# Kernel tuning notes

Hardware: AMD Instinct MI355X
Metric: run time of the kernel (lower is better)

## Reference

```python
import jax, jax.numpy as jnp
import numpy as np

GATE_THRESH = 0.4
LN_EPS = 1e-5
NORM_EPS = 1e-12  # torch F.normalize eps


def setup_inputs() -> dict:
    key = jax.random.key(0)
    ks = jax.random.split(key, 8)
    B, L, H, V = 64, 1024, 64, 32000
    s = lambda k, shape, scale: (jax.random.normal(k, shape, jnp.float32) * scale)
    return {
        "seq": jax.random.randint(ks[0], (B, L), 0, V),
        "embed": s(ks[1], (V, H), 0.02),
        "W1": s(ks[2], (H, 2 * H), 0.05), "b1": jnp.zeros((2 * H,), jnp.float32),
        "W2": s(ks[3], (2 * H, H), 0.05), "b2": jnp.zeros((H,), jnp.float32),
        "gamma": jnp.ones((H,), jnp.float32), "beta": jnp.zeros((H,), jnp.float32),
        "kpW": s(ks[4], (H, H), 0.1),
        "rpW": s(ks[5], (H, H), 0.1), "rpb": jnp.zeros((H,), jnp.float32),
        "outW": s(ks[6], (H, V), 0.05), "outb": jnp.zeros((V,), jnp.float32),
    }


def reference(seq, embed, W1, b1, W2, b2, gamma, beta, kpW, rpW, rpb, outW, outb):
    # embed + FF residual + LayerNorm
    h = embed[seq]                                        # (B,L,H)
    ffo = jax.nn.relu(h @ W1 + b1) @ W2 + b2
    x = h + ffo
    mu = x.mean(-1, keepdims=True)
    var = x.var(-1, keepdims=True)                        # biased, like torch LN
    h = (x - mu) * jax.lax.rsqrt(var + LN_EPS) * gamma + beta

    k_all = h @ kpW                                       # kp projection for all t, (B,L,H)
    B, L, H = h.shape

    def step(M, k):                                       # M: (B,H,H), k: (B,H)
        kn = k / jnp.maximum(jnp.linalg.norm(k, axis=-1, keepdims=True), NORM_EPS)
        vp = jnp.einsum('bij,bj->bi', M, kn)
        err = k - vp
        gate = (jnp.linalg.norm(err, axis=-1) >= GATE_THRESH * jnp.linalg.norm(k, axis=-1)).astype(k.dtype)
        Delta = gate[:, None, None] * err[:, :, None] * kn[:, None, :]
        return M + Delta, None                            # use_ema=False -> plain accumulation

    M0 = jnp.zeros((B, H, H), h.dtype)
    M, _ = jax.lax.scan(step, M0, jnp.swapaxes(k_all[:, :-1], 0, 1))  # scan over L-1 steps

    q = k_all[:, -1]                                      # query from last token
    read = jnp.einsum('bij,bj->bi', M, q)
    return (read @ rpW + rpb) @ outW + outb               # (B,V)
```

## Files before the change

### kernel.cpp

```cpp
#include <hip/hip_runtime.h>
#include <hip/hip_bf16.h>

#define HDIM 64
#define LSEQ 1024
#define NB 64
#define NV 32000
#define CC 32
#define NCH 32
#define NT (NB * LSEQ)

template<int CTRL>
__device__ __forceinline__ float dpp_red(float x) {
  int y = __builtin_amdgcn_update_dpp(0, __float_as_int(x), CTRL, 0xF, 0xF, true);
  return x + __int_as_float(y);
}
__device__ __forceinline__ float quad_sum(float x) {
  x = dpp_red<0xB1>(x);
  x = dpp_red<0x4E>(x);
  return x;
}
__device__ __forceinline__ float wave_sum(float x) {
  x = dpp_red<0xB1>(x);
  x = dpp_red<0x4E>(x);
  x = dpp_red<0x141>(x);
  x = dpp_red<0x140>(x);
  float a = __int_as_float(__builtin_amdgcn_readlane(__float_as_int(x), 0));
  float b = __int_as_float(__builtin_amdgcn_readlane(__float_as_int(x), 16));
  float c = __int_as_float(__builtin_amdgcn_readlane(__float_as_int(x), 32));
  float d = __int_as_float(__builtin_amdgcn_readlane(__float_as_int(x), 48));
  return (a + b) + (c + d);
}

__global__ __launch_bounds__(256) void transpose_w(const float* __restrict__ W1,
    const float* __restrict__ kpW, float* __restrict__ W1T, float* __restrict__ kpWT)
{
  const int tid = blockIdx.x * 256 + threadIdx.x;
  if (tid < 8192) { const int c = tid >> 6, j = tid & 63; W1T[tid] = W1[j * 128 + c]; }
  else { const int e = tid - 8192; const int i = e >> 6, j = e & 63; kpWT[e] = kpW[j * 64 + i]; }
}

__global__ __launch_bounds__(256, 1) void tok4(
    const int* __restrict__ seq, const float* __restrict__ embed,
    const float* __restrict__ W1T, const float* __restrict__ b1,
    const float* __restrict__ W2, const float* __restrict__ b2,
    const float* __restrict__ gamma, const float* __restrict__ beta,
    const float* __restrict__ kpWT, float* __restrict__ kallT,
    float* __restrict__ thr2_all, float* __restrict__ inv_all)
{
  const int tok = blockIdx.x * 256 + threadIdx.x;
  const int row = seq[tok];
  float h[64], x[64];
  const float4* ep = (const float4*)(embed + (size_t)row * HDIM);
  #pragma unroll
  for (int q = 0; q < 16; ++q) {
    const float4 v = ep[q];
    h[4*q] = v.x; h[4*q+1] = v.y; h[4*q+2] = v.z; h[4*q+3] = v.w;
  }
  #pragma unroll
  for (int j = 0; j < 64; ++j) x[j] = h[j] + b2[j];

  for (int c = 0; c < 128; ++c) {
    const float* w1r = W1T + c * 64;
    float a0 = 0.f, a1 = 0.f, a2 = 0.f, a3 = 0.f;
    #pragma unroll
    for (int j = 0; j < 64; j += 4) {
      a0 = fmaf(h[j],   w1r[j],   a0);
      a1 = fmaf(h[j+1], w1r[j+1], a1);
      a2 = fmaf(h[j+2], w1r[j+2], a2);
      a3 = fmaf(h[j+3], w1r[j+3], a3);
    }
    const float y = fmaxf(b1[c] + ((a0 + a1) + (a2 + a3)), 0.f);
    const float* w2r = W2 + c * 64;
    #pragma unroll
    for (int j = 0; j < 64; ++j) x[j] = fmaf(y, w2r[j], x[j]);
  }

  float s0=0.f,s1=0.f,s2=0.f,s3=0.f,q0=0.f,q1=0.f,q2=0.f,q3=0.f;
  #pragma unroll
  for (int j = 0; j < 64; j += 4) {
    s0 += x[j]; s1 += x[j+1]; s2 += x[j+2]; s3 += x[j+3];
    q0 = fmaf(x[j],   x[j],   q0); q1 = fmaf(x[j+1], x[j+1], q1);
    q2 = fmaf(x[j+2], x[j+2], q2); q3 = fmaf(x[j+3], x[j+3], q3);
  }
  const float mu  = ((s0+s1)+(s2+s3)) * (1.f/64.f);
  const float var = ((q0+q1)+(q2+q3)) * (1.f/64.f) - mu * mu;
  const float rs  = rsqrtf(var + 1e-5f);
  #pragma unroll
  for (int j = 0; j < 64; ++j) h[j] = (x[j] - mu) * rs * gamma[j] + beta[j];

  float nk2 = 0.f;
  for (int i = 0; i < 64; ++i) {
    const float* kr = kpWT + i * 64;
    float c0=0.f,c1=0.f,c2=0.f,c3=0.f;
    #pragma unroll
    for (int j = 0; j < 64; j += 4) {
      c0 = fmaf(h[j],   kr[j],   c0);
      c1 = fmaf(h[j+1], kr[j+1], c1);
      c2 = fmaf(h[j+2], kr[j+2], c2);
      c3 = fmaf(h[j+3], kr[j+3], c3);
    }
    const float ki = (c0 + c1) + (c2 + c3);
    nk2 = fmaf(ki, ki, nk2);
    kallT[(size_t)i * NT + tok] = ki;
  }
  thr2_all[tok] = 0.16f * nk2;
  inv_all[tok]  = 1.f / fmaxf(sqrtf(nk2), 1e-12f);
}

__global__ __launch_bounds__(64) void gram2(const float* __restrict__ kallT,
    const float* __restrict__ inv_all, float* __restrict__ Gg)
{
  const int bi = blockIdx.x;
  const int b = bi >> 5, ch = bi & 31;
  const int l = threadIdx.x;
  const int t0 = (l & 7) * 4, s0 = (l >> 3) * 4;
  const size_t gb = (size_t)b * LSEQ + ch * CC;
  float g00=0,g01=0,g02=0,g03=0, g10=0,g11=0,g12=0,g13=0;
  float g20=0,g21=0,g22=0,g23=0, g30=0,g31=0,g32=0,g33=0;
  for (int j = 0; j < 64; ++j) {
    const float* rowp = kallT + (size_t)j * NT + gb;
    const float4 a = *(const float4*)(rowp + t0);
    const float4 c = *(const float4*)(rowp + s0);
    g00=fmaf(a.x,c.x,g00); g01=fmaf(a.x,c.y,g01); g02=fmaf(a.x,c.z,g02); g03=fmaf(a.x,c.w,g03);
    g10=fmaf(a.y,c.x,g10); g11=fmaf(a.y,c.y,g11); g12=fmaf(a.y,c.z,g12); g13=fmaf(a.y,c.w,g13);
    g20=fmaf(a.z,c.x,g20); g21=fmaf(a.z,c.y,g21); g22=fmaf(a.z,c.z,g22); g23=fmaf(a.z,c.w,g23);
    g30=fmaf(a.w,c.x,g30); g31=fmaf(a.w,c.y,g31); g32=fmaf(a.w,c.z,g32); g33=fmaf(a.w,c.w,g33);
  }
  const float4 it = *(const float4*)(inv_all + gb + t0);
  const float4 is = *(const float4*)(inv_all + gb + s0);
  float* Go = Gg + (size_t)bi * (CC * CC);
  float4 o;
  o.x=g00*it.x*is.x; o.y=g01*it.x*is.y; o.z=g02*it.x*is.z; o.w=g03*it.x*is.w;
  *(float4*)(Go + (t0+0)*CC + s0) = o;
  o.x=g10*it.y*is.x; o.y=g11*it.y*is.y; o.z=g12*it.y*is.z; o.w=g13*it.y*is.w;
  *(float4*)(Go + (t0+1)*CC + s0) = o;
  o.x=g20*it.z*is.x; o.y=g21*it.z*is.y; o.z=g22*it.z*is.z; o.w=g23*it.z*is.w;
  *(float4*)(Go + (t0+2)*CC + s0) = o;
  o.x=g30*it.w*is.x; o.y=g31*it.w*is.y; o.z=g32*it.w*is.z; o.w=g33*it.w*is.w;
  *(float4*)(Go + (t0+3)*CC + s0) = o;
}

__global__ __launch_bounds__(192, 1) void scan6(
    const float* __restrict__ kallT, const float* __restrict__ thr2_all,
    const float* __restrict__ inv_all, const float* __restrict__ Gg,
    float* __restrict__ readv)
{
  __shared__ float kS[3][CC * 68];
  __shared__ float GS[2][CC * CC];
  __shared__ float rS[CC * 64];
  __shared__ float cstS[CC * 64];
  __shared__ float thr2S[2][CC];
  __shared__ float invS[3][CC];

  const int b = blockIdx.x, tid = threadIdx.x;
  const int w = tid >> 6, l = tid & 63;
  const int A = l >> 2, B4 = l & 3;
  const int r0 = 32 * (w - 1) + 2 * A;
  const int jb = 16 * B4;
  const size_t gbase = (size_t)b * LSEQ;

  float M0[16], M1[16], acc[32];
  #pragma unroll
  for (int q = 0; q < 16; ++q) { M0[q] = 0.f; M1[q] = 0.f; }

#define A2_SLICE(KB, IB, T0) do {                                              \
    _Pragma("unroll")                                                          \
    for (int t = (T0); t < (T0) + 8; ++t) {                                    \
      const float* kr = &kS[KB][t * 68 + jb];                                  \
      float p0a=0.f,p0b=0.f,p1a=0.f,p1b=0.f;                                   \
      _Pragma("unroll")                                                        \
      for (int q2 = 0; q2 < 4; ++q2) {                                         \
        const float4 kv = ((const float4*)kr)[q2];                             \
        p0a = fmaf(M0[4*q2+0], kv.x, p0a); p0b = fmaf(M0[4*q2+1], kv.y, p0b);  \
        p0a = fmaf(M0[4*q2+2], kv.z, p0a); p0b = fmaf(M0[4*q2+3], kv.w, p0b);  \
        p1a = fmaf(M1[4*q2+0], kv.x, p1a); p1b = fmaf(M1[4*q2+1], kv.y, p1b);  \
        p1a = fmaf(M1[4*q2+2], kv.z, p1a); p1b = fmaf(M1[4*q2+3], kv.w, p1b);  \
      }                                                                        \
      float p0 = quad_sum(p0a + p0b);                                          \
      float p1 = quad_sum(p1a + p1b);                                          \
      const float iv = invS[IB][t];                                            \
      if (B4 == 0) *(float2*)&rS[t * 64 + r0] = make_float2(p0 * iv, p1 * iv); \
    }                                                                          \
  } while (0)

#define C_SLICE(KB, IB, S0) do {                                               \
    _Pragma("unroll")                                                          \
    for (int s = (S0); s < (S0) + 8; ++s) {                                    \
      const float2 cc2 = *(const float2*)&cstS[s * 64 + r0];                   \
      const float iv = invS[IB][s];                                            \
      const float c0 = cc2.x * iv, c1 = cc2.y * iv;                            \
      const float* kr = &kS[KB][s * 68 + jb];                                  \
      _Pragma("unroll")                                                        \
      for (int q2 = 0; q2 < 4; ++q2) {                                         \
        const float4 kv = ((const float4*)kr)[q2];                             \
        M0[4*q2+0] = fmaf(c0, kv.x, M0[4*q2+0]); M0[4*q2+1] = fmaf(c0, kv.y, M0[4*q2+1]); \
        M0[4*q2+2] = fmaf(c0, kv.z, M0[4*q2+2]); M0[4*q2+3] = fmaf(c0, kv.w, M0[4*q2+3]); \
        M1[4*q2+0] = fmaf(c1, kv.x, M1[4*q2+0]); M1[4*q2+1] = fmaf(c1, kv.y, M1[4*q2+1]); \
        M1[4*q2+2] = fmaf(c1, kv.z, M1[4*q2+2]); M1[4*q2+3] = fmaf(c1, kv.w, M1[4*q2+3]); \
      }                                                                        \
    }                                                                          \
  } while (0)

#define B_SLICE(Q, CBUF, CGI, LASTCH) do {                                     \
    const int t0_ = 8 * (Q);                                                   \
    _Pragma("unroll")                                                          \
    for (int i = 0; i < 8; ++i) {                                              \
      const int u = t0_ + i;                                                   \
      acc[u] += kS[CBUF][u * 68 + l] - rS[u * 64 + l];                         \
    }                                                                          \
    const float4 tha = ((const float4*)&thr2S[CGI][t0_])[0];                   \
    const float4 thb = ((const float4*)&thr2S[CGI][t0_])[1];                   \
    const float th8[8] = {tha.x,tha.y,tha.z,tha.w, thb.x,thb.y,thb.z,thb.w};   \
    _Pragma("unroll")                                                          \
    for (int i = 0; i < 8; ++i) {                                              \
      const int t = t0_ + i;                                                   \
      float g[32];                                                             \
      const float4* gp = (const float4*)&GS[CGI][t * 32];                      \
      _Pragma("unroll")                                                        \
      for (int r = 0; r < 8; ++r) {                                            \
        const float4 v = gp[r];                                                \
        g[4*r]=v.x; g[4*r+1]=v.y; g[4*r+2]=v.z; g[4*r+3]=v.w;                  \
      }                                                                        \
      const float err = acc[t];                                                \
      const float ne2 = wave_sum(err * err);                                   \
      bool gate = (ne2 >= th8[i]);                                             \
      if ((LASTCH) && t == CC - 1) gate = false;                               \
      const float c = gate ? err : 0.f;                                        \
      cstS[t * 64 + l] = c;                                                    \
      _Pragma("unroll")                                                        \
      for (int u = 0; u < 32; ++u) acc[u] = fmaf(-g[u], c, acc[u]);            \
    }                                                                          \
  } while (0)

  if (w < 2) {
    const float* src = kallT + (size_t)l * NT + gbase + w * 16;
    #pragma unroll
    for (int q = 0; q < 4; ++q) {
      const float4 v = ((const float4*)src)[q];
      const int t0 = w * 16 + q * 4;
      kS[0][(t0+0)*68 + l] = v.x; kS[0][(t0+1)*68 + l] = v.y;
      kS[0][(t0+2)*68 + l] = v.z; kS[0][(t0+3)*68 + l] = v.w;
    }
  } else {
    const float4* gsrc = (const float4*)(Gg + (size_t)b * NCH * (CC * CC));
    #pragma unroll
    for (int q = 0; q < 4; ++q) ((float4*)GS[0])[q * 64 + l] = gsrc[q * 64 + l];
    if (l < CC) thr2S[0][l] = thr2_all[gbase + l];
    else        invS[0][l - CC] = inv_all[gbase + (l - CC)];
  }
  __syncthreads();

  for (int ch = 0; ch < NCH; ++ch) {
    const int cb = ch % 3, pb = (ch + 2) % 3, nb = (ch + 1) % 3;
    const int cg = ch & 1, ng = 1 - cg;
    const bool lastch = (ch == NCH - 1);

    if (w == 0) {
      #pragma unroll
      for (int u = 0; u < 32; ++u) acc[u] = 0.f;
      if (!lastch) {
        const float* src = kallT + (size_t)l * NT + gbase + (ch + 1) * CC;
        #pragma unroll
        for (int q = 0; q < 8; ++q) {
          const float4 v = ((const float4*)src)[q];
          const int t0 = q * 4;
          kS[nb][(t0+0)*68 + l] = v.x; kS[nb][(t0+1)*68 + l] = v.y;
          kS[nb][(t0+2)*68 + l] = v.z; kS[nb][(t0+3)*68 + l] = v.w;
        }
        const float4* gsrc = (const float4*)(Gg + ((size_t)b * NCH + ch + 1) * (CC * CC));
        #pragma unroll
        for (int q = 0; q < 4; ++q) ((float4*)GS[ng])[q * 64 + l] = gsrc[q * 64 + l];
        if (l < CC) thr2S[ng][l] = thr2_all[gbase + (ch + 1) * CC + l];
        else        invS[nb][l - CC] = inv_all[gbase + (ch + 1) * CC + (l - CC)];
      }
    } else {
      if (ch > 0) C_SLICE(pb, pb, 24);
      A2_SLICE(cb, cb, 0);
    }
    __syncthreads();

    if (w == 0) B_SLICE(0, cb, cg, lastch);
    else        A2_SLICE(cb, cb, 8);
    __syncthreads();
    if (w == 0) B_SLICE(1, cb, cg, lastch);
    else        A2_SLICE(cb, cb, 16);
    __syncthreads();
    if (w == 0) B_SLICE(2, cb, cg, lastch);
    else { A2_SLICE(cb, cb, 24); C_SLICE(cb, cb, 0); }
    __syncthreads();
    if (w == 0) B_SLICE(3, cb, cg, lastch);
    else { C_SLICE(cb, cb, 8); C_SLICE(cb, cb, 16); }
    __syncthreads();
  }

  {
    constexpr int fb = (NCH - 1) % 3;
    if (w > 0) {
      C_SLICE(fb, fb, 24);
      const float* kr = &kS[fb][(CC - 1) * 68 + jb];
      float p0a=0.f,p0b=0.f,p1a=0.f,p1b=0.f;
      #pragma unroll
      for (int q2 = 0; q2 < 4; ++q2) {
        const float4 kv = ((const float4*)kr)[q2];
        p0a = fmaf(M0[4*q2+0], kv.x, p0a); p0b = fmaf(M0[4*q2+1], kv.y, p0b);
        p0a = fmaf(M0[4*q2+2], kv.z, p0a); p0b = fmaf(M0[4*q2+3], kv.w, p0b);
        p1a = fmaf(M1[4*q2+0], kv.x, p1a); p1b = fmaf(M1[4*q2+1], kv.y, p1b);
        p1a = fmaf(M1[4*q2+2], kv.z, p1a); p1b = fmaf(M1[4*q2+3], kv.w, p1b);
      }
      float d0 = quad_sum(p0a + p0b);
      float d1 = quad_sum(p1a + p1b);
      if (B4 == 0) *(float2*)&readv[b * 64 + r0] = make_float2(d0, d1);
    }
  }
#undef A2_SLICE
#undef C_SLICE
#undef B_SLICE
}

__global__ __launch_bounds__(64) void rproj_kernel(const float* __restrict__ readv,
    const float* __restrict__ rpW, const float* __restrict__ rpb, float* __restrict__ r2T)
{
  const int b = blockIdx.x, i = threadIdx.x;
  const float* rv = readv + b * 64;
  float acc = rpb[i];
  #pragma unroll
  for (int j = 0; j < 64; ++j)
    acc = fmaf(rv[j], rpW[j * 64 + i], acc);
  r2T[i * 64 + b] = acc;
}

__global__ __launch_bounds__(256, 1) void out_kernel(const float* __restrict__ r2T,
    const float* __restrict__ outW, const float* __restrict__ outb,
    float* __restrict__ out)
{
  const int v = blockIdx.x * 256 + threadIdx.x;
  float acc[64];
  #pragma unroll
  for (int b = 0; b < 64; ++b) acc[b] = 0.f;
  for (int k = 0; k < 64; ++k) {
    const float wv = outW[(size_t)k * NV + v];
    const float* rr = r2T + k * 64;
    #pragma unroll
    for (int b = 0; b < 64; ++b)
      acc[b] = fmaf(rr[b], wv, acc[b]);
  }
  const float ob = outb[v];
  #pragma unroll
  for (int b = 0; b < 64; ++b)
    out[(size_t)b * NV + v] = acc[b] + ob;
}

extern "C" void kernel_launch(void* const* d_in, const int* in_sizes, int n_in,
                              void* d_out, int out_size, void* d_ws, size_t ws_size,
                              hipStream_t stream)
{
  const int*   seq   = (const int*)d_in[0];
  const float* embed = (const float*)d_in[1];
  const float* W1    = (const float*)d_in[2];
  const float* b1    = (const float*)d_in[3];
  const float* W2    = (const float*)d_in[4];
  const float* b2    = (const float*)d_in[5];
  const float* gam   = (const float*)d_in[6];
  const float* bet   = (const float*)d_in[7];
  const float* kpW   = (const float*)d_in[8];
  const float* rpW   = (const float*)d_in[9];
  const float* rpb   = (const float*)d_in[10];
  const float* outW  = (const float*)d_in[11];
  const float* outb  = (const float*)d_in[12];
  float* out = (float*)d_out;

  float* ws = (float*)d_ws;
  float* kallT = ws;
  float* G     = kallT + (size_t)HDIM * NT;
  float* thr2  = G     + (size_t)NB * NCH * CC * CC;
  float* inv   = thr2  + NT;
  float* readv = inv   + NT;
  float* r2T   = readv + NB * HDIM;
  float* W1T   = r2T   + NB * HDIM;
  float* kpWT  = W1T   + 8192;

  hipLaunchKernelGGL(transpose_w, dim3(48), dim3(256), 0, stream, W1, kpW, W1T, kpWT);
  hipLaunchKernelGGL(tok4, dim3(256), dim3(256), 0, stream,
                     seq, embed, W1T, b1, W2, b2, gam, bet, kpWT, kallT, thr2, inv);
  hipLaunchKernelGGL(gram2, dim3(NB * NCH), dim3(64), 0, stream, kallT, inv, G);
  hipLaunchKernelGGL(scan6, dim3(NB), dim3(192), 0, stream, kallT, thr2, inv, G, readv);
  hipLaunchKernelGGL(rproj_kernel, dim3(NB), dim3(64), 0, stream, readv, rpW, rpb, r2T);
  hipLaunchKernelGGL(out_kernel, dim3(NV / 256), dim3(256), 0, stream, r2T, outW, outb, out);
}
```

Measured before the change: 485.5 us.

## Pipeline gate reduction in scan slice and shrink output kernel blocks

Restructures the per-step gating loop in the sequential scan. The next step's error is updated and reduced before the remaining accumulator updates, so the wave reduction latency overlaps with the FMA work. Gram rows are double-buffered and loaded one step ahead, and updates skip triangular entries that no longer matter. The wave sum now uses row-broadcast DPP with a single readlane instead of four readlanes. Separately, the output projection kernel uses 128-thread blocks to spread its 250 blocks across more CUs. This adds register pressure and more complex control flow in the scan.

```diff
diff --git a/kernel.cpp b/kernel.cpp
--- a/kernel.cpp
+++ b/kernel.cpp
@@ -19,16 +19,14 @@
   x = dpp_red<0x4E>(x);
   return x;
 }
-__device__ __forceinline__ float wave_sum(float x) {
+__device__ __forceinline__ float wave_sum63(float x) {
   x = dpp_red<0xB1>(x);
   x = dpp_red<0x4E>(x);
   x = dpp_red<0x141>(x);
   x = dpp_red<0x140>(x);
-  float a = __int_as_float(__builtin_amdgcn_readlane(__float_as_int(x), 0));
-  float b = __int_as_float(__builtin_amdgcn_readlane(__float_as_int(x), 16));
-  float c = __int_as_float(__builtin_amdgcn_readlane(__float_as_int(x), 32));
-  float d = __int_as_float(__builtin_amdgcn_readlane(__float_as_int(x), 48));
-  return (a + b) + (c + d);
+  x = dpp_red<0x142>(x);
+  x = dpp_red<0x143>(x);
+  return x;
 }
 
 __global__ __launch_bounds__(256) void transpose_w(const float* __restrict__ W1,
@@ -203,32 +201,49 @@
 
 #define B_SLICE(Q, CBUF, CGI, LASTCH) do {                                     \
     const int t0_ = 8 * (Q);                                                   \
+    float kr_[8], rr_[8];                                                      \
     _Pragma("unroll")                                                          \
     for (int i = 0; i < 8; ++i) {                                              \
-      const int u = t0_ + i;                                                   \
-      acc[u] += kS[CBUF][u * 68 + l] - rS[u * 64 + l];                         \
+      kr_[i] = kS[CBUF][(t0_ + i) * 68 + l];                                   \
+      rr_[i] = rS[(t0_ + i) * 64 + l];                                         \
     }                                                                          \
     const float4 tha = ((const float4*)&thr2S[CGI][t0_])[0];                   \
     const float4 thb = ((const float4*)&thr2S[CGI][t0_])[1];                   \
     const float th8[8] = {tha.x,tha.y,tha.z,tha.w, thb.x,thb.y,thb.z,thb.w};   \
+    float g2_[2][32];                                                          \
+    _Pragma("unroll")                                                          \
+    for (int q = (t0_ + 1) >> 2; q < 8; ++q) {                                 \
+      const float4 v = ((const float4*)&GS[CGI][t0_ * 32])[q];                 \
+      g2_[0][4*q+0] = v.x; g2_[0][4*q+1] = v.y;                                \
+      g2_[0][4*q+2] = v.z; g2_[0][4*q+3] = v.w;                                \
+    }                                                                          \
+    float err_ = acc[t0_] + kr_[0] - rr_[0];                                   \
+    float red_ = wave_sum63(err_ * err_);                                      \
     _Pragma("unroll")                                                          \
     for (int i = 0; i < 8; ++i) {                                              \
       const int t = t0_ + i;                                                   \
-      float g[32];                                                             \
-      const float4* gp = (const float4*)&GS[CGI][t * 32];                      \
+      if (i < 7) {                                                             \
+        _Pragma("unroll")                                                      \
+        for (int q = (t + 2) >> 2; q < 8; ++q) {                               \
+          const float4 v = ((const float4*)&GS[CGI][(t + 1) * 32])[q];         \
+          g2_[(i+1)&1][4*q+0] = v.x; g2_[(i+1)&1][4*q+1] = v.y;                \
+          g2_[(i+1)&1][4*q+2] = v.z; g2_[(i+1)&1][4*q+3] = v.w;                \
+        }                                                                      \
+      }                                                                        \
+      const float ne2_ = __int_as_float(                                       \
+          __builtin_amdgcn_readlane(__float_as_int(red_), 63));                \
+      bool gate_ = (ne2_ >= th8[i]);                                           \
+      if ((LASTCH) && t == CC - 1) gate_ = false;                              \
+      const float c = gate_ ? err_ : 0.f;                                      \
+      cstS[t * 64 + l] = c;                                                    \
+      if (i < 7) {                                                             \
+        acc[t + 1] = fmaf(-g2_[i & 1][t + 1], c, acc[t + 1]);                  \
+        err_ = acc[t + 1] + kr_[i + 1] - rr_[i + 1];                           \
+        red_ = wave_sum63(err_ * err_);                                        \
+      }                                                                        \
       _Pragma("unroll")                                                        \
-      for (int r = 0; r < 8; ++r) {                                            \
-        const float4 v = gp[r];                                                \
-        g[4*r]=v.x; g[4*r+1]=v.y; g[4*r+2]=v.z; g[4*r+3]=v.w;                  \
-      }                                                                        \
-      const float err = acc[t];                                                \
-      const float ne2 = wave_sum(err * err);                                   \
-      bool gate = (ne2 >= th8[i]);                                             \
-      if ((LASTCH) && t == CC - 1) gate = false;                               \
-      const float c = gate ? err : 0.f;                                        \
-      cstS[t * 64 + l] = c;                                                    \
-      _Pragma("unroll")                                                        \
-      for (int u = 0; u < 32; ++u) acc[u] = fmaf(-g[u], c, acc[u]);            \
+      for (int u = (i < 7) ? (t + 2) : (t + 1); u < CC; ++u)                   \
+        acc[u] = fmaf(-g2_[i & 1][u], c, acc[u]);                              \
     }                                                                          \
   } while (0)
 
@@ -329,11 +344,11 @@
   r2T[i * 64 + b] = acc;
 }
 
-__global__ __launch_bounds__(256, 1) void out_kernel(const float* __restrict__ r2T,
+__global__ __launch_bounds__(128, 1) void out_kernel(const float* __restrict__ r2T,
     const float* __restrict__ outW, const float* __restrict__ outb,
     float* __restrict__ out)
 {
-  const int v = blockIdx.x * 256 + threadIdx.x;
+  const int v = blockIdx.x * 128 + threadIdx.x;
   float acc[64];
   #pragma unroll
   for (int b = 0; b < 64; ++b) acc[b] = 0.f;
@@ -385,5 +400,5 @@
   hipLaunchKernelGGL(gram2, dim3(NB * NCH), dim3(64), 0, stream, kallT, inv, G);
   hipLaunchKernelGGL(scan6, dim3(NB), dim3(192), 0, stream, kallT, thr2, inv, G, readv);
   hipLaunchKernelGGL(rproj_kernel, dim3(NB), dim3(64), 0, stream, readv, rpW, rpb, r2T);
-  hipLaunchKernelGGL(out_kernel, dim3(NV / 256), dim3(256), 0, stream, r2T, outW, outb, out);
-}
+  hipLaunchKernelGGL(out_kernel, dim3(NV / 128), dim3(128), 0, stream, r2T, outW, outb, out);
+}
```

Result: no change. 477.6 us (-1.6%).
